# Optimization experiments

Hardware: AMD Instinct MI355X
Metric: run time of the kernel (lower is better)

The kernel has to match this reference:

```python
import jax, jax.numpy as jnp
import numpy as np

D_IN = 1024
D_OUT = 1024
NUM_HEADS = 16
HEAD_DIM = D_OUT // NUM_HEADS
CONTEXT_LEN = 2048


def setup_inputs() -> dict:
    key = jax.random.key(0)
    ks = jax.random.split(key, 7)
    scale = 0.02
    x = jax.random.normal(ks[0], (2, 2048, D_IN), dtype=jnp.float32)
    Wq = jax.random.normal(ks[1], (D_IN, D_OUT), dtype=jnp.float32) * scale
    bq = jnp.zeros((D_OUT,), dtype=jnp.float32)
    Wk = jax.random.normal(ks[2], (D_IN, D_OUT), dtype=jnp.float32) * scale
    bk = jnp.zeros((D_OUT,), dtype=jnp.float32)
    Wv = jax.random.normal(ks[3], (D_IN, D_OUT), dtype=jnp.float32) * scale
    bv = jnp.zeros((D_OUT,), dtype=jnp.float32)
    return {"x": x, "Wq": Wq, "bq": bq, "Wk": Wk, "bk": bk, "Wv": Wv, "bv": bv}


def reference(x, Wq, bq, Wk, bk, Wv, bv):
    B, S, _ = x.shape
    # QKV projections with bias
    q = x @ Wq + bq  # [B,S,D_OUT]
    k = x @ Wk + bk
    v = x @ Wv + bv
    # split heads -> [B,H,S,Dh]
    def heads(t):
        return t.reshape(B, S, NUM_HEADS, HEAD_DIM).transpose(0, 2, 1, 3)
    q, k, v = heads(q), heads(k), heads(v)
    # raw scores, then additive causal mask (-1e9 on strictly upper triangle),
    # then scale by 1/sqrt(head_dim) AFTER adding mask (matches original code)
    scores = jnp.einsum("bhqd,bhkd->bhqk", q, k)
    causal = jnp.tril(jnp.ones((S, S), dtype=bool))
    add_mask = jnp.where(causal, 0.0, -1e9).astype(scores.dtype)
    scores = scores + add_mask
    weights = jax.nn.softmax(scores / jnp.sqrt(jnp.asarray(HEAD_DIM, scores.dtype)), axis=-1)
    ctx = jnp.einsum("bhqk,bhkd->bhqd", weights, v)  # [B,H,S,Dh]
    return ctx.transpose(0, 2, 1, 3).reshape(B, S, D_OUT)
```

## Files before the change

### kernel.cpp

```cpp
#include <hip/hip_runtime.h>
#include <hip/hip_bf16.h>
#include <stdint.h>

#define D_IN 1024
#define NH 16
#define DH 64
#define SEQ 2048
#define BATCH 2

typedef unsigned short u16;
typedef __attribute__((ext_vector_type(8))) short short8;
typedef __attribute__((ext_vector_type(4))) float f32x4;

#define CSCALE 0.1803368801f

__device__ __forceinline__ u16 f2bf(float f) {
    union { float f; uint32_t u; } v; v.f = f;
    uint32_t r = v.u + 0x7FFF + ((v.u >> 16) & 1);
    return (u16)(r >> 16);
}

__device__ __forceinline__ float bf2f(u16 u) {
    union { uint32_t u; float f; } v; v.u = (uint32_t)u << 16;
    return v.f;
}

__device__ __forceinline__ uint32_t pktrunc(float a, float b) {
    union { float f; uint32_t u; } x, y;
    x.f = a; y.f = b;
    return __builtin_amdgcn_perm(y.u, x.u, 0x07060302u);
}

__device__ __forceinline__ void async16(const u16* g, u16* l) {
    __builtin_amdgcn_global_load_lds(
        (const __attribute__((address_space(1))) void*)g,
        (__attribute__((address_space(3))) void*)l, 16, 0, 0);
}

__global__ __launch_bounds__(256) void prep_kernel(
    const float* __restrict__ x, const float* __restrict__ Wq,
    const float* __restrict__ Wk, const float* __restrict__ Wv,
    u16* __restrict__ xb, u16* __restrict__ WT)
{
    __shared__ float tile[64][65];
    if (blockIdx.x < 4096) {
        int i = (blockIdx.x * 256 + threadIdx.x) * 4;
        float4 v = *(const float4*)(x + i);
        union { u16 u[4]; uint2 d; } o;
        o.u[0] = f2bf(v.x); o.u[1] = f2bf(v.y); o.u[2] = f2bf(v.z); o.u[3] = f2bf(v.w);
        *(uint2*)(xb + i) = o.d;
        return;
    }
    int idx = blockIdx.x - 4096;
    int mat = idx >> 8, rem = idx & 255;
    int k0 = (rem & 15) * 64, n0 = (rem >> 4) * 64;
    const float* W = (mat == 0) ? Wq : (mat == 1 ? Wk : Wv);
    int c = threadIdx.x & 63, rb = threadIdx.x >> 6;
    #pragma unroll
    for (int p = 0; p < 16; ++p) {
        int r = p * 4 + rb;
        tile[r][c] = W[(size_t)(k0 + r) * 1024 + n0 + c];
    }
    __syncthreads();
    #pragma unroll
    for (int p = 0; p < 16; ++p) {
        int r = p * 4 + rb;
        WT[((size_t)mat * 1024 + n0 + r) * 1024 + k0 + c] = f2bf(tile[c][r]);
    }
}

__global__ __launch_bounds__(256) void qkv_gemm_kernel(
    const u16* __restrict__ xb, const u16* __restrict__ WT,
    const float* __restrict__ bq, const float* __restrict__ bk,
    const float* __restrict__ bv,
    u16* __restrict__ Qb, u16* __restrict__ Kb, u16* __restrict__ Vt)
{
    __shared__ u16 smem[4 * 64 * 72];
    u16* As = smem;
    u16* Bs = smem + 128 * 64;
    const int tid  = threadIdx.x;
    const int wave = tid >> 6, lane = tid & 63;
    const int quad = lane >> 4, l15 = lane & 15;
    const int m0 = blockIdx.y * 128;
    const int n0 = blockIdx.x * 128;

    f32x4 acc[4][4];
    #pragma unroll
    for (int i = 0; i < 4; ++i)
        #pragma unroll
        for (int j = 0; j < 4; ++j)
            acc[i][j] = (f32x4){0.f, 0.f, 0.f, 0.f};

    const int wm = wave & 1, wn = wave >> 1;
    const int srow8 = tid >> 3;
    const int sslot = tid & 7;
    const int fsig  = l15 & 7;

    for (int k0 = 0; k0 < 1024; k0 += 64) {
        #pragma unroll
        for (int rnd = 0; rnd < 4; ++rnd) {
            int row = rnd * 32 + srow8;
            int g = sslot ^ (row & 7);
            async16(xb + (size_t)(m0 + row) * 1024 + k0 + g * 8, As + rnd * 2048 + tid * 8);
            async16(WT + (size_t)(n0 + row) * 1024 + k0 + g * 8, Bs + rnd * 2048 + tid * 8);
        }
        __syncthreads();
        #pragma unroll
        for (int kk = 0; kk < 2; ++kk) {
            short8 af[4], bfr[4];
            #pragma unroll
            for (int f = 0; f < 4; ++f) {
                int slot = ((kk << 2) + quad) ^ fsig;
                af[f]  = *(const short8*)(As + (wm * 64 + f * 16 + l15) * 64 + slot * 8);
                bfr[f] = *(const short8*)(Bs + (wn * 64 + f * 16 + l15) * 64 + slot * 8);
            }
            #pragma unroll
            for (int i = 0; i < 4; ++i)
                #pragma unroll
                for (int j = 0; j < 4; ++j)
                    acc[i][j] = __builtin_amdgcn_mfma_f32_16x16x32_bf16(af[i], bfr[j], acc[i][j], 0, 0, 0);
        }
        __syncthreads();
    }

    const int mat = n0 >> 10;
    const int ncb = (n0 & 1023) + wn * 64;
    const int hh = ncb >> 6;
    const int bb = m0 >> 11, sb = m0 & 2047;

    if (mat < 2) {
        const float* bias = (mat == 0) ? bq : bk;
        u16* dst = (mat == 0) ? Qb : Kb;
        const float sc = (mat == 0) ? CSCALE : 1.0f;
        #pragma unroll
        for (int i = 0; i < 4; ++i) {
            int ss = sb + wm * 64 + i * 16 + quad * 4;
            #pragma unroll
            for (int j = 0; j < 4; ++j) {
                int dh = j * 16 + l15;
                float bval = bias[ncb + dh];
                size_t base = (((size_t)bb * NH + hh) * SEQ + ss) * DH + dh;
                #pragma unroll
                for (int r = 0; r < 4; ++r)
                    dst[base + (size_t)r * DH] = f2bf((acc[i][j][r] + bval) * sc);
            }
        }
    } else {
        u16* vt = smem + wave * (64 * 72);
        #pragma unroll
        for (int i = 0; i < 4; ++i)
            #pragma unroll
            for (int j = 0; j < 4; ++j) {
                float bval = bv[ncb + j * 16 + l15];
                union { u16 u[4]; uint2 d; } o;
                #pragma unroll
                for (int r = 0; r < 4; ++r)
                    o.u[r] = f2bf(acc[i][j][r] + bval);
                *(uint2*)(vt + (j * 16 + l15) * 72 + i * 16 + quad * 4) = o.d;
            }
        const int s0w = sb + wm * 64;
        u16* vdst = Vt + ((size_t)(bb * NH + hh) * DH) * SEQ;
        #pragma unroll
        for (int it = 0; it < 8; ++it) {
            int dh = it * 8 + (lane >> 3);
            short8 v = *(const short8*)(vt + dh * 72 + (lane & 7) * 8);
            *(short8*)(vdst + (size_t)dh * SEQ + s0w + (lane & 7) * 8) = v;
        }
    }
}

__device__ __forceinline__ void stage64(const u16* g0, size_t gstride, u16* lds,
                                        int wave, int lane)
{
    #pragma unroll
    for (int rnd = 0; rnd < 2; ++rnd) {
        int row = rnd * 32 + wave * 8 + (lane >> 3);
        int sig = ((row >> 3) & 1) * 4 + (row & 3);
        int c = (lane & 7) ^ sig;
        async16(g0 + (size_t)row * gstride + c * 8, lds + row * 64 + (lane & 7) * 8);
    }
}

__global__ __launch_bounds__(256) void flash_mfma_kernel(
    const u16* __restrict__ Qb, const u16* __restrict__ Kb,
    const u16* __restrict__ Vt, float* __restrict__ out,
    u16* __restrict__ Opart, float* __restrict__ Lpart)
{
    static const int JQT[24] = {7,15,15,14,14, 6,13,13,12,12, 5,11,11,10,10,
                                4, 9, 9, 8, 8, 3, 2, 1, 0};
    static const int JHF[24] = {-1,0,1,0,1, -1,0,1,0,1, -1,0,1,0,1,
                                -1,0,1,0,1, -1,-1,-1,-1};

    __shared__ u16 Ks[2][64 * 64];
    __shared__ u16 Vs[2][64 * 64];

    const int tid  = threadIdx.x;
    const int wave = tid >> 6, lane = tid & 63;
    const int quad = lane >> 4, l15 = lane & 15;
    const int bhx = blockIdx.x;
    const int b = bhx >> 4, h = bhx & 15;
    const int job = blockIdx.y;
    const int qt = JQT[job], hf = JHF[job];
    const int t0 = (hf == 1) ? qt + 1 : 0;
    const int t1 = (hf == 0) ? qt + 1 : 2 * qt + 2;
    const int q0 = qt * 128;
    const int wq0 = wave * 32;
    const size_t bh = (size_t)bhx;
    const u16* Qp = Qb + bh * SEQ * DH;
    const u16* Kp = Kb + bh * SEQ * DH;
    const u16* Vp = Vt + bh * DH * SEQ;

    short8 qf[2][2];
    #pragma unroll
    for (int qa = 0; qa < 2; ++qa) {
        const u16* qrp = Qp + (size_t)(q0 + wq0 + qa * 16 + l15) * DH;
        qf[qa][0] = *(const short8*)(qrp + quad * 8);
        qf[qa][1] = *(const short8*)(qrp + 32 + quad * 8);
    }

    const short8 ones = (short8){0x3F80, 0x3F80, 0x3F80, 0x3F80,
                                 0x3F80, 0x3F80, 0x3F80, 0x3F80};

    f32x4 O[2][4], L[2];
    #pragma unroll
    for (int pa = 0; pa < 2; ++pa) {
        #pragma unroll
        for (int f = 0; f < 4; ++f) O[pa][f] = (f32x4){0.f, 0.f, 0.f, 0.f};
        L[pa] = (f32x4){0.f, 0.f, 0.f, 0.f};
    }

    const int wqmax = q0 + wq0 + 31;
    const int krbase = (l15 >> 2) * 8 + (l15 & 3);
    const int ksig   = ((l15 >> 2) & 1) * 4 + (l15 & 3);
    const int vsig   = ((l15 >> 3) & 1) * 4 + (l15 & 3);

    stage64(Kp + (size_t)t0 * 64 * DH, DH, Ks[t0 & 1], wave, lane);
    stage64(Vp + t0 * 64, SEQ, Vs[t0 & 1], wave, lane);
    __syncthreads();

    for (int t = t0; t < t1; ++t) {
        const int cur = t & 1;
        if (t + 1 < t1) {
            int k1 = (t + 1) * 64;
            stage64(Kp + (size_t)k1 * DH, DH, Ks[cur ^ 1], wave, lane);
            stage64(Vp + k1, SEQ, Vs[cur ^ 1], wave, lane);
        }
        const int k0 = t * 64;
        if (k0 <= wqmax) {
            f32x4 sf[4][2];
            #pragma unroll
            for (int fj = 0; fj < 4; ++fj) {
                int krow = (fj >> 1) * 32 + krbase + (fj & 1) * 4;
                const u16* kp = &Ks[cur][krow * 64];
                short8 k0f = *(const short8*)(kp + (quad ^ ksig) * 8);
                short8 k1f = *(const short8*)(kp + ((4 + quad) ^ ksig) * 8);
                #pragma unroll
                for (int qa = 0; qa < 2; ++qa) {
                    f32x4 s = (f32x4){0.f, 0.f, 0.f, 0.f};
                    s = __builtin_amdgcn_mfma_f32_16x16x32_bf16(k0f, qf[qa][0], s, 0, 0, 0);
                    s = __builtin_amdgcn_mfma_f32_16x16x32_bf16(k1f, qf[qa][1], s, 0, 0, 0);
                    sf[fj][qa] = s;
                }
            }
            const bool diag = (k0 + 63 > q0 + wq0);
            short8 pA[2][2];
            #pragma unroll
            for (int qa = 0; qa < 2; ++qa) {
                #pragma unroll
                for (int fj = 0; fj < 4; ++fj)
                    #pragma unroll
                    for (int r = 0; r < 4; ++r) {
                        float p = __builtin_amdgcn_exp2f(sf[fj][qa][r]);
                        if (diag) {
                            int key = k0 + (fj >> 1) * 32 + quad * 8 + (fj & 1) * 4 + r;
                            int qg  = q0 + wq0 + qa * 16 + l15;
                            p = (key <= qg) ? p : 0.f;
                        }
                        sf[fj][qa][r] = p;
                    }
                union { uint32_t d[4]; short8 v; } a0, a1;
                a0.d[0] = pktrunc(sf[0][qa][0], sf[0][qa][1]);
                a0.d[1] = pktrunc(sf[0][qa][2], sf[0][qa][3]);
                a0.d[2] = pktrunc(sf[1][qa][0], sf[1][qa][1]);
                a0.d[3] = pktrunc(sf[1][qa][2], sf[1][qa][3]);
                a1.d[0] = pktrunc(sf[2][qa][0], sf[2][qa][1]);
                a1.d[1] = pktrunc(sf[2][qa][2], sf[2][qa][3]);
                a1.d[2] = pktrunc(sf[3][qa][0], sf[3][qa][1]);
                a1.d[3] = pktrunc(sf[3][qa][2], sf[3][qa][3]);
                pA[qa][0] = a0.v;
                pA[qa][1] = a1.v;
                L[qa] = __builtin_amdgcn_mfma_f32_16x16x32_bf16(pA[qa][0], ones, L[qa], 0, 0, 0);
                L[qa] = __builtin_amdgcn_mfma_f32_16x16x32_bf16(pA[qa][1], ones, L[qa], 0, 0, 0);
            }
            #pragma unroll
            for (int fo = 0; fo < 4; ++fo) {
                const u16* vrow = &Vs[cur][(fo * 16 + l15) * 64];
                short8 vb0 = *(const short8*)(vrow + (quad ^ vsig) * 8);
                short8 vb1 = *(const short8*)(vrow + ((4 + quad) ^ vsig) * 8);
                #pragma unroll
                for (int pa = 0; pa < 2; ++pa) {
                    O[pa][fo] = __builtin_amdgcn_mfma_f32_16x16x32_bf16(pA[pa][0], vb0, O[pa][fo], 0, 0, 0);
                    O[pa][fo] = __builtin_amdgcn_mfma_f32_16x16x32_bf16(pA[pa][1], vb1, O[pa][fo], 0, 0, 0);
                }
            }
        }
        __syncthreads();
    }

    if (hf < 0) {
        #pragma unroll
        for (int pa = 0; pa < 2; ++pa)
            #pragma unroll
            for (int fo = 0; fo < 4; ++fo)
                #pragma unroll
                for (int r = 0; r < 4; ++r) {
                    int s = q0 + wq0 + pa * 16 + quad * 4 + r;
                    out[((size_t)b * SEQ + s) * 1024 + h * DH + fo * 16 + l15] =
                        O[pa][fo][r] / L[pa][r];
                }
    } else {
        const int pi = (qt - 8) * 2 + hf;
        u16* op = Opart + (((size_t)pi * 32 + bhx) * 128) * 64;
        float* lp = Lpart + ((size_t)pi * 32 + bhx) * 128;
        #pragma unroll
        for (int pa = 0; pa < 2; ++pa) {
            #pragma unroll
            for (int fo = 0; fo < 4; ++fo)
                #pragma unroll
                for (int r = 0; r < 4; ++r) {
                    int ql = wq0 + pa * 16 + quad * 4 + r;
                    op[(size_t)ql * 64 + fo * 16 + l15] = f2bf(O[pa][fo][r]);
                }
            if (l15 == 0) {
                #pragma unroll
                for (int r = 0; r < 4; ++r)
                    lp[wq0 + pa * 16 + quad * 4 + r] = L[pa][r];
            }
        }
    }
}

__global__ __launch_bounds__(256) void combine_kernel(
    const u16* __restrict__ Opart, const float* __restrict__ Lpart,
    float* __restrict__ out)
{
    int blk = blockIdx.x;
    int qt = 8 + (blk >> 5);
    int bh = blk & 31;
    int b = bh >> 4, h = bh & 15;
    int pi0 = (qt - 8) * 2, pi1 = pi0 + 1;
    int tid = threadIdx.x;
    int q = tid >> 1, seg = (tid & 1) * 32;
    const u16* o0 = Opart + (((size_t)pi0 * 32 + bh) * 128 + q) * 64 + seg;
    const u16* o1 = Opart + (((size_t)pi1 * 32 + bh) * 128 + q) * 64 + seg;
    float inv = 1.0f / (Lpart[((size_t)pi0 * 32 + bh) * 128 + q] +
                        Lpart[((size_t)pi1 * 32 + bh) * 128 + q]);
    float* op = out + ((size_t)b * SEQ + qt * 128 + q) * 1024 + h * DH + seg;
    #pragma unroll
    for (int d = 0; d < 32; d += 4) {
        union { uint2 d2; u16 u[4]; } a, c;
        a.d2 = *(const uint2*)(o0 + d);
        c.d2 = *(const uint2*)(o1 + d);
        float4 v;
        v.x = (bf2f(a.u[0]) + bf2f(c.u[0])) * inv;
        v.y = (bf2f(a.u[1]) + bf2f(c.u[1])) * inv;
        v.z = (bf2f(a.u[2]) + bf2f(c.u[2])) * inv;
        v.w = (bf2f(a.u[3]) + bf2f(c.u[3])) * inv;
        *(float4*)(op + d) = v;
    }
}

extern "C" void kernel_launch(void* const* d_in, const int* in_sizes, int n_in,
                              void* d_out, int out_size, void* d_ws, size_t ws_size,
                              hipStream_t stream) {
    const float* x  = (const float*)d_in[0];
    const float* Wq = (const float*)d_in[1];
    const float* bq = (const float*)d_in[2];
    const float* Wk = (const float*)d_in[3];
    const float* bk = (const float*)d_in[4];
    const float* Wv = (const float*)d_in[5];
    const float* bv = (const float*)d_in[6];
    float* out = (float*)d_out;

    const size_t NX = (size_t)BATCH * SEQ * D_IN;
    const size_t NW = (size_t)3 * D_IN * 1024;
    const size_t NP = (size_t)BATCH * NH * SEQ * DH;
    u16* xb = (u16*)d_ws;
    u16* WT = xb + NX;
    u16* Qb = WT + NW;
    u16* Kb = Qb + NP;
    u16* Vt = Kb + NP;
    u16* Opart = xb;
    float* Lpart = (float*)(xb + NX);

    prep_kernel<<<4096 + 768, 256, 0, stream>>>(x, Wq, Wk, Wv, xb, WT);
    qkv_gemm_kernel<<<dim3(24, 32), 256, 0, stream>>>(xb, WT, bq, bk, bv, Qb, Kb, Vt);
    flash_mfma_kernel<<<dim3(32, 24), 256, 0, stream>>>(Qb, Kb, Vt, out, Opart, Lpart);
    combine_kernel<<<256, 256, 0, stream>>>(Opart, Lpart, out);
}
```

Baseline: 162.6 us.

## Rewrite QKV GEMM with 256x256 tiles, double-buffered async pipeline and block swizzle

The QKV projection GEMM now uses 512-thread blocks computing 256x256 output tiles, launched as 192 blocks on a 1D grid. The linear block index is remapped so tiles are grouped across XCDs. K-slices go into double-buffered LDS, and loads for step t+2 are issued inside the MFMA loop, with waves paced by barriers, vmcnt waits and s_setprio. The goal is to hide global-load latency and raise reuse per loaded tile, at the cost of a grid that may not cover every CU and higher LDS and register pressure.

```diff
diff --git a/kernel.cpp b/kernel.cpp
--- a/kernel.cpp
+++ b/kernel.cpp
@@ -69,59 +69,111 @@
     }
 }
 
-__global__ __launch_bounds__(256) void qkv_gemm_kernel(
+__global__ __launch_bounds__(512, 2) void qkv_gemm_kernel(
     const u16* __restrict__ xb, const u16* __restrict__ WT,
     const float* __restrict__ bq, const float* __restrict__ bk,
     const float* __restrict__ bv,
     u16* __restrict__ Qb, u16* __restrict__ Kb, u16* __restrict__ Vt)
 {
-    __shared__ u16 smem[4 * 64 * 72];
+    __shared__ u16 smem[65536];
     u16* As = smem;
-    u16* Bs = smem + 128 * 64;
+    u16* Bs = smem + 32768;
+
     const int tid  = threadIdx.x;
     const int wave = tid >> 6, lane = tid & 63;
     const int quad = lane >> 4, l15 = lane & 15;
-    const int m0 = blockIdx.y * 128;
-    const int n0 = blockIdx.x * 128;
-
-    f32x4 acc[4][4];
-    #pragma unroll
-    for (int i = 0; i < 4; ++i)
+    const int wm = wave >> 2, wn = wave & 3;
+    const int fsig = l15 & 7;
+
+    const int lin = blockIdx.x;
+    const int logical = (lin & 7) * 24 + (lin >> 3);
+    const int by = logical / 12;
+    const int bx = logical % 12;
+    const int m0 = by * 256;
+    const int n0 = bx * 256;
+
+    const int ch  = tid & 7;
+    const int rwT = tid >> 3;
+
+    f32x4 acc[8][4];
+    #pragma unroll
+    for (int i = 0; i < 8; ++i)
         #pragma unroll
         for (int j = 0; j < 4; ++j)
             acc[i][j] = (f32x4){0.f, 0.f, 0.f, 0.f};
 
-    const int wm = wave & 1, wn = wave >> 1;
-    const int srow8 = tid >> 3;
-    const int sslot = tid & 7;
-    const int fsig  = l15 & 7;
-
-    for (int k0 = 0; k0 < 1024; k0 += 64) {
-        #pragma unroll
-        for (int rnd = 0; rnd < 4; ++rnd) {
-            int row = rnd * 32 + srow8;
-            int g = sslot ^ (row & 7);
-            async16(xb + (size_t)(m0 + row) * 1024 + k0 + g * 8, As + rnd * 2048 + tid * 8);
-            async16(WT + (size_t)(n0 + row) * 1024 + k0 + g * 8, Bs + rnd * 2048 + tid * 8);
-        }
-        __syncthreads();
-        #pragma unroll
-        for (int kk = 0; kk < 2; ++kk) {
-            short8 af[4], bfr[4];
-            #pragma unroll
-            for (int f = 0; f < 4; ++f) {
-                int slot = ((kk << 2) + quad) ^ fsig;
-                af[f]  = *(const short8*)(As + (wm * 64 + f * 16 + l15) * 64 + slot * 8);
-                bfr[f] = *(const short8*)(Bs + (wn * 64 + f * 16 + l15) * 64 + slot * 8);
-            }
-            #pragma unroll
-            for (int i = 0; i < 4; ++i)
-                #pragma unroll
-                for (int j = 0; j < 4; ++j)
-                    acc[i][j] = __builtin_amdgcn_mfma_f32_16x16x32_bf16(af[i], bfr[j], acc[i][j], 0, 0, 0);
-        }
-        __syncthreads();
-    }
+    auto stageA = [&](int buf, int kst) {
+        #pragma unroll
+        for (int r = 0; r < 4; ++r) {
+            int row = r * 64 + rwT;
+            int g = ch ^ (row & 7);
+            async16(xb + (size_t)(m0 + row) * 1024 + kst + g * 8,
+                    As + buf * 16384 + row * 64 + ch * 8);
+        }
+    };
+    auto stageBh = [&](int buf, int kst, int half) {
+        #pragma unroll
+        for (int r = 0; r < 2; ++r) {
+            int row = half * 128 + r * 64 + rwT;
+            int g = ch ^ (row & 7);
+            async16(WT + (size_t)(n0 + row) * 1024 + kst + g * 8,
+                    Bs + buf * 16384 + row * 64 + ch * 8);
+        }
+    };
+
+    stageA(0, 0);  stageBh(0, 0, 0);  stageBh(0, 0, 1);
+    stageA(1, 64); stageBh(1, 64, 0); stageBh(1, 64, 1);
+    asm volatile("s_waitcnt vmcnt(8)" ::: "memory");
+    __builtin_amdgcn_sched_barrier(0);
+    __builtin_amdgcn_s_barrier();
+
+    for (int t = 0; t < 16; ++t) {
+        const int cur = t & 1;
+        const u16* Ab = As + cur * 16384;
+        const u16* Bb = Bs + cur * 16384;
+        const bool st = (t + 2 < 16);
+        const int k2 = (t + 2) * 64;
+
+        short8 bfr[4][2];
+        #pragma unroll
+        for (int j = 0; j < 4; ++j)
+            #pragma unroll
+            for (int kk = 0; kk < 2; ++kk)
+                bfr[j][kk] = *(const short8*)(Bb + (wn * 64 + j * 16 + l15) * 64 +
+                                              (((kk << 2) + quad) ^ fsig) * 8);
+
+        #pragma unroll
+        for (int p = 0; p < 4; ++p) {
+            short8 af[2][2];
+            #pragma unroll
+            for (int i2 = 0; i2 < 2; ++i2)
+                #pragma unroll
+                for (int kk = 0; kk < 2; ++kk)
+                    af[i2][kk] = *(const short8*)(Ab + (wm * 128 + (p * 2 + i2) * 16 + l15) * 64 +
+                                                  (((kk << 2) + quad) ^ fsig) * 8);
+            if (p == 1 && st) stageBh(cur, k2, 0);
+            if (p == 2 && st) stageBh(cur, k2, 1);
+            __builtin_amdgcn_s_barrier();
+            if (p == 3 && st) stageA(cur, k2);
+            __builtin_amdgcn_s_setprio(1);
+            #pragma unroll
+            for (int kk = 0; kk < 2; ++kk)
+                #pragma unroll
+                for (int i2 = 0; i2 < 2; ++i2)
+                    #pragma unroll
+                    for (int j = 0; j < 4; ++j)
+                        acc[p * 2 + i2][j] = __builtin_amdgcn_mfma_f32_16x16x32_bf16(
+                            af[i2][kk], bfr[j][kk], acc[p * 2 + i2][j], 0, 0, 0);
+            __builtin_amdgcn_s_setprio(0);
+            if (p == 3) {
+                if (st)            { asm volatile("s_waitcnt vmcnt(8)" ::: "memory"); }
+                else if (t == 14)  { asm volatile("s_waitcnt vmcnt(0)" ::: "memory"); }
+                __builtin_amdgcn_sched_barrier(0);
+            }
+            __builtin_amdgcn_s_barrier();
+        }
+    }
+    __syncthreads();
 
     const int mat = n0 >> 10;
     const int ncb = (n0 & 1023) + wn * 64;
@@ -133,8 +185,8 @@
         u16* dst = (mat == 0) ? Qb : Kb;
         const float sc = (mat == 0) ? CSCALE : 1.0f;
         #pragma unroll
-        for (int i = 0; i < 4; ++i) {
-            int ss = sb + wm * 64 + i * 16 + quad * 4;
+        for (int i = 0; i < 8; ++i) {
+            int ss = sb + wm * 128 + i * 16 + quad * 4;
             #pragma unroll
             for (int j = 0; j < 4; ++j) {
                 int dh = j * 16 + l15;
@@ -147,24 +199,27 @@
         }
     } else {
         u16* vt = smem + wave * (64 * 72);
-        #pragma unroll
-        for (int i = 0; i < 4; ++i)
-            #pragma unroll
-            for (int j = 0; j < 4; ++j) {
-                float bval = bv[ncb + j * 16 + l15];
-                union { u16 u[4]; uint2 d; } o;
-                #pragma unroll
-                for (int r = 0; r < 4; ++r)
-                    o.u[r] = f2bf(acc[i][j][r] + bval);
-                *(uint2*)(vt + (j * 16 + l15) * 72 + i * 16 + quad * 4) = o.d;
-            }
-        const int s0w = sb + wm * 64;
         u16* vdst = Vt + ((size_t)(bb * NH + hh) * DH) * SEQ;
         #pragma unroll
-        for (int it = 0; it < 8; ++it) {
-            int dh = it * 8 + (lane >> 3);
-            short8 v = *(const short8*)(vt + dh * 72 + (lane & 7) * 8);
-            *(short8*)(vdst + (size_t)dh * SEQ + s0w + (lane & 7) * 8) = v;
+        for (int h2 = 0; h2 < 2; ++h2) {
+            #pragma unroll
+            for (int i = 0; i < 4; ++i)
+                #pragma unroll
+                for (int j = 0; j < 4; ++j) {
+                    float bval = bv[ncb + j * 16 + l15];
+                    union { u16 u[4]; uint2 d; } o;
+                    #pragma unroll
+                    for (int r = 0; r < 4; ++r)
+                        o.u[r] = f2bf(acc[h2 * 4 + i][j][r] + bval);
+                    *(uint2*)(vt + (j * 16 + l15) * 72 + i * 16 + quad * 4) = o.d;
+                }
+            const int s0w = sb + wm * 128 + h2 * 64;
+            #pragma unroll
+            for (int it = 0; it < 8; ++it) {
+                int dh = it * 8 + (lane >> 3);
+                short8 v = *(const short8*)(vt + dh * 72 + (lane & 7) * 8);
+                *(short8*)(vdst + (size_t)dh * SEQ + s0w + (lane & 7) * 8) = v;
+            }
         }
     }
 }
@@ -394,7 +449,7 @@
     float* Lpart = (float*)(xb + NX);
 
     prep_kernel<<<4096 + 768, 256, 0, stream>>>(x, Wq, Wk, Wv, xb, WT);
-    qkv_gemm_kernel<<<dim3(24, 32), 256, 0, stream>>>(xb, WT, bq, bk, bv, Qb, Kb, Vt);
+    qkv_gemm_kernel<<<dim3(192), 512, 0, stream>>>(xb, WT, bq, bk, bv, Qb, Kb, Vt);
     flash_mfma_kernel<<<dim3(32, 24), 256, 0, stream>>>(Qb, Kb, Vt, out, Opart, Lpart);
     combine_kernel<<<256, 256, 0, stream>>>(Opart, Lpart, out);
 }
```

New measurement: 156.2 us. -4.0%, faster.
